# Kernel tuning notes

Measured on AMD Instinct MI355X. Metric: run time of the kernel, lower is better.

Reference implementation:

```python
import jax, jax.numpy as jnp
import numpy as np

CH = 256
B, H, W = 8, 128, 128
CQK = CH // 8


def _conv1x1(x, w, b):
    # x: [B,C,H,W], w: [O,C], b: [O]
    return jnp.einsum('bchw,oc->bohw', x, w) + b[None, :, None, None]


def setup_inputs() -> dict:
    key = jax.random.key(0)
    ks = jax.random.split(key, 8)
    sq = 1.0 / np.sqrt(CH)
    return {
        'x': jax.random.normal(ks[0], (B, CH, H, W), dtype=jnp.float32),
        'Wq': jax.random.normal(ks[1], (CQK, CH), dtype=jnp.float32) * sq,
        'bq': jax.random.normal(ks[2], (CQK,), dtype=jnp.float32) * 0.01,
        'Wk': jax.random.normal(ks[3], (CQK, CH), dtype=jnp.float32) * sq,
        'bk': jax.random.normal(ks[4], (CQK,), dtype=jnp.float32) * 0.01,
        'Wv': jax.random.normal(ks[5], (CH, CH), dtype=jnp.float32) * sq,
        'bv': jax.random.normal(ks[6], (CH,), dtype=jnp.float32) * 0.01,
        'gamma': jax.random.normal(ks[7], (1,), dtype=jnp.float32) * 0.1,
        'recurrence': 2,
    }


def reference(x, Wq, bq, Wk, bk, Wv, bv, gamma, recurrence):
    q = _conv1x1(x, Wq, bq)   # [B, C//8, H, W]
    k = _conv1x1(x, Wk, bk)   # [B, C//8, H, W]
    v = _conv1x1(x, Wv, bv)   # [B, C, H, W]
    if recurrence % 2 == 1:
        # attention along W, independently per (b, h); no mask
        energy = jnp.einsum('bchi,bchj->bhij', q, k)      # [B,H,W,W]
        att = jax.nn.softmax(energy, axis=-1)
        out = jnp.einsum('bchj,bhij->bchi', v, att)       # [B,C,H,W]
    else:
        # attention along H, independently per (b, w); diagonal masked -inf
        energy = jnp.einsum('bciw,bcjw->bwij', q, k)      # [B,W,H,H]
        h = energy.shape[-1]
        diag = jnp.eye(h, dtype=bool)[None, None]
        energy = jnp.where(diag, -jnp.inf, energy)
        att = jax.nn.softmax(energy, axis=-1)             # [B,W,H,H]
        out = jnp.einsum('bcjw,bwij->bciw', v, att)       # [B,C,H,W]
    return gamma[0] * out + x
```

## Files before the change

### kernel.cpp

```cpp
#include <hip/hip_runtime.h>
#include <hip/hip_bf16.h>

#define B_   8
#define CH_  256
#define CQK_ 32
#define H_   128
#define W_   128

typedef __attribute__((ext_vector_type(8))) short s16x8;
typedef __attribute__((ext_vector_type(4))) float f32x4;
typedef __attribute__((ext_vector_type(4))) unsigned short u16x4;

__device__ __forceinline__ unsigned short f2b(float f) {
  __hip_bfloat16 h = __float2bfloat16(f);
  return *(unsigned short*)&h;
}
__device__ __forceinline__ float b2f(unsigned short u) {
  return __uint_as_float(((unsigned)u) << 16);
}


__global__ void kw_pack(const float* __restrict__ Wq, const float* __restrict__ Wk,
                        const float* __restrict__ Wv, unsigned short* __restrict__ wqk,
                        unsigned short* __restrict__ wv) {
  int idx = blockIdx.x * 256 + threadIdx.x;
  if (idx < 64 * 256) {
    int qc = idx >> 8, c = idx & 255;
    wqk[idx] = f2b(qc < 32 ? Wq[qc * 256 + c] : Wk[(qc - 32) * 256 + c]);
  } else {
    int i2 = idx - 64 * 256;
    wv[i2] = f2b(Wv[i2]);
  }
}

__global__ __launch_bounds__(256) void k0_xpose(const float* __restrict__ x,
                                                unsigned short* __restrict__ xt) {
  __shared__ unsigned short st[256 * 137];
  const int t = threadIdx.x;
  const int b = blockIdx.x >> 7;
  const int h = blockIdx.x & 127;
  const float* xin = x + ((size_t)b * 256 * 128 + h) * 128;
  const int w = t & 127, chalf = t >> 7;
#pragma unroll 8
  for (int it = 0; it < 128; ++it) {
    int c = it * 2 + chalf;
    st[c * 137 + w] = f2b(xin[(size_t)c * 16384 + w]);
  }
  __syncthreads();
  unsigned short* xo = xt + ((size_t)b * 128 * 128 + h) * 256;
  const int cl = t & 127, whalf = t >> 7;
#pragma unroll 8
  for (int it = 0; it < 64; ++it) {
    int wr = it * 2 + whalf;
    unsigned v = (unsigned)st[(2 * cl) * 137 + wr] |
                 ((unsigned)st[(2 * cl + 1) * 137 + wr] << 16);
    *(unsigned*)&xo[(size_t)wr * 32768 + 2 * cl] = v;
  }
}

__global__ __launch_bounds__(256, 2) void k0b_xpose(const unsigned short* __restrict__ xt,
                                                    unsigned short* __restrict__ xt2) {
  __shared__ unsigned short st[128 * 264];
  const int t = threadIdx.x;
  const size_t colbase = (size_t)blockIdx.x * 32768;
#pragma unroll
  for (int it = 0; it < 16; ++it) {
    int ch = it * 256 + t;
    int row = ch >> 5, off = (ch & 31) * 8;
    *(uint4*)&st[row * 264 + off] = *(const uint4*)&xt[colbase + ch * 8];
  }
  __syncthreads();
  const int hpl = t & 3, cq = t >> 2;
#pragma unroll 8
  for (int it = 0; it < 64; ++it) {
    const int itc = it & 3, ith = it >> 2;
    const int c = itc * 64 + cq;
    const int hp = ith * 4 + hpl;
    unsigned v = (unsigned)st[(2 * hp) * 264 + c] |
                 ((unsigned)st[(2 * hp + 1) * 264 + c] << 16);
    *(unsigned*)&xt2[colbase + (size_t)c * 128 + hp * 2] = v;
  }
}

__device__ __forceinline__ void gld_lds16(const unsigned short* g, unsigned short* l) {
  __builtin_amdgcn_global_load_lds(
      (const __attribute__((address_space(1))) void*)g,
      (__attribute__((address_space(3))) void*)l, 16, 0, 0);
}

__device__ __forceinline__ void stage_tile(const unsigned short* __restrict__ gsrc,
                                           unsigned short* lds, int k0,
                                           int wv_id, int lane) {
#pragma unroll
  for (int i = 0; i < 4; ++i) {
    const int chunk = wv_id * 4 + i;
    const int L = chunk * 1024 + lane * 16;
    const int row = L >> 7;
    const int sb = L & 127;
    const int srcb = sb ^ ((row & 7) << 4);
    gld_lds16(gsrc + row * 256 + k0 + (srcb >> 1), lds + chunk * 512);
  }
}

struct SmemY {
  unsigned short qt[128 * 40];
  unsigned short kt[128 * 40];
  union {
    unsigned short att[128 * 136];
    unsigned short xstage[2][128 * 64];
  } u;
};

__global__ __launch_bounds__(256, 2)
void k1y(const unsigned short* __restrict__ xt, const unsigned short* __restrict__ xt2,
         const unsigned short* __restrict__ wqk, const float* __restrict__ bq,
         const float* __restrict__ bk, unsigned short* __restrict__ y) {
  __shared__ SmemY sm;
  const int t = threadIdx.x;
  const int wvid = t >> 6;
  const int lane = t & 63;
  const int l15 = lane & 15;
  const int quad = lane >> 4;
  const int b = blockIdx.x >> 7;
  const int w = blockIdx.x & 127;
  const size_t colbase = ((size_t)b * 128 + w) * 32768;

  {
    const int qc0 = wvid * 16;
    f32x4 acc[8];
#pragma unroll
    for (int nt = 0; nt < 8; ++nt) acc[nt] = {0.f, 0.f, 0.f, 0.f};
    const unsigned short* arow = wqk + (qc0 + l15) * 256 + quad * 8;
    const unsigned short* gcol = xt + colbase;
    stage_tile(gcol, sm.u.xstage[0], 0, wvid, lane);
    __syncthreads();
#pragma unroll
    for (int kc = 0; kc < 4; ++kc) {
      const int cur = kc & 1;
      if (kc < 3) stage_tile(gcol, sm.u.xstage[cur ^ 1], (kc + 1) * 64, wvid, lane);
#pragma unroll
      for (int kk2 = 0; kk2 < 2; ++kk2) {
        s16x8 a = *(const s16x8*)(arow + (kc * 2 + kk2) * 32);
#pragma unroll
        for (int nt = 0; nt < 8; ++nt) {
          const int row = nt * 16 + l15;
          const int col = (kk2 * 64 + quad * 16) ^ ((row & 7) << 4);
          s16x8 bb = *(const s16x8*)((const char*)sm.u.xstage[cur] + row * 128 + col);
          acc[nt] = __builtin_amdgcn_mfma_f32_16x16x32_bf16(a, bb, acc[nt], 0, 0, 0);
        }
      }
      __syncthreads();
    }
    const float* bp = (wvid < 2) ? bq : bk;
    const int qcl = qc0 & 16;
    float bias[4];
#pragma unroll
    for (int r = 0; r < 4; ++r) bias[r] = bp[qcl + quad * 4 + r];
    unsigned short* dst = (wvid < 2) ? sm.qt : sm.kt;
#pragma unroll
    for (int nt = 0; nt < 8; ++nt) {
      int h = nt * 16 + l15;
      u16x4 pk;
#pragma unroll
      for (int r = 0; r < 4; ++r) pk[r] = f2b(acc[nt][r] + bias[r]);
      *(u16x4*)&dst[h * 40 + qcl + quad * 4] = pk;
    }
  }
  __syncthreads();

  s16x8 bXpf[4][4];
  {
    const int c0 = wvid * 64;
#pragma unroll
    for (int kj = 0; kj < 4; ++kj)
#pragma unroll
      for (int nt = 0; nt < 4; ++nt)
        bXpf[kj][nt] = *(const s16x8*)&xt2[colbase + (size_t)(c0 + nt * 16 + l15) * 128 +
                                            kj * 32 + quad * 8];
  }
  __builtin_amdgcn_sched_barrier(0);

  {
    const int i0 = wvid * 32;
    s16x8 aQ[2];
#pragma unroll
    for (int mt = 0; mt < 2; ++mt)
      aQ[mt] = *(const s16x8*)&sm.qt[(i0 + mt * 16 + l15) * 40 + quad * 8];
    f32x4 eacc[2][8];
#pragma unroll
    for (int mt = 0; mt < 2; ++mt)
#pragma unroll
      for (int nt = 0; nt < 8; ++nt) eacc[mt][nt] = {0.f, 0.f, 0.f, 0.f};
#pragma unroll
    for (int nt = 0; nt < 8; ++nt) {
      s16x8 bK = *(const s16x8*)&sm.kt[(nt * 16 + l15) * 40 + quad * 8];
      eacc[0][nt] = __builtin_amdgcn_mfma_f32_16x16x32_bf16(aQ[0], bK, eacc[0][nt], 0, 0, 0);
      eacc[1][nt] = __builtin_amdgcn_mfma_f32_16x16x32_bf16(aQ[1], bK, eacc[1][nt], 0, 0, 0);
    }
#pragma unroll
    for (int mt = 0; mt < 2; ++mt)
#pragma unroll
      for (int nt = 0; nt < 8; ++nt) {
        const int j = nt * 16 + l15;
#pragma unroll
        for (int r = 0; r < 4; ++r)
          if (j == i0 + mt * 16 + quad * 4 + r) eacc[mt][nt][r] = -__builtin_inff();
      }
#pragma unroll
    for (int mt = 0; mt < 2; ++mt)
#pragma unroll
      for (int r = 0; r < 4; ++r) {
        float mx = -__builtin_inff();
#pragma unroll
        for (int nt = 0; nt < 8; ++nt) mx = fmaxf(mx, eacc[mt][nt][r]);
        mx = fmaxf(mx, __shfl_xor(mx, 1));
        mx = fmaxf(mx, __shfl_xor(mx, 2));
        mx = fmaxf(mx, __shfl_xor(mx, 4));
        mx = fmaxf(mx, __shfl_xor(mx, 8));
        float s = 0.f;
#pragma unroll
        for (int nt = 0; nt < 8; ++nt) {
          float p = __expf(eacc[mt][nt][r] - mx);
          eacc[mt][nt][r] = p;
          s += p;
        }
        s += __shfl_xor(s, 1);
        s += __shfl_xor(s, 2);
        s += __shfl_xor(s, 4);
        s += __shfl_xor(s, 8);
        const float inv = 1.0f / s;
        const int i = i0 + mt * 16 + quad * 4 + r;
#pragma unroll
        for (int nt = 0; nt < 8; ++nt)
          sm.u.att[i * 136 + nt * 16 + l15] = f2b(eacc[mt][nt][r] * inv);
      }
  }
  __syncthreads();

  f32x4 yacc[8][4];
#pragma unroll
  for (int mt = 0; mt < 8; ++mt)
#pragma unroll
    for (int nt = 0; nt < 4; ++nt) yacc[mt][nt] = {0.f, 0.f, 0.f, 0.f};
  {
#pragma unroll
    for (int kj = 0; kj < 4; ++kj) {
      s16x8 aP[8];
#pragma unroll
      for (int mt = 0; mt < 8; ++mt)
        aP[mt] = *(const s16x8*)&sm.u.att[(mt * 16 + l15) * 136 + kj * 32 + quad * 8];
#pragma unroll
      for (int nt = 0; nt < 4; ++nt) {
#pragma unroll
        for (int mt = 0; mt < 8; ++mt)
          yacc[mt][nt] = __builtin_amdgcn_mfma_f32_16x16x32_bf16(aP[mt], bXpf[kj][nt],
                                                                 yacc[mt][nt], 0, 0, 0);
      }
    }
  }
#pragma unroll 1
  for (int h2 = 0; h2 < 2; ++h2) {
    __syncthreads();
    if ((wvid >> 1) == h2) {
      const int clb = (wvid & 1) * 64;
#pragma unroll
      for (int mt = 0; mt < 8; ++mt)
#pragma unroll
        for (int nt = 0; nt < 4; ++nt) {
          const int cl = clb + nt * 16 + l15;
#pragma unroll
          for (int r = 0; r < 4; ++r)
            sm.u.att[(mt * 16 + quad * 4 + r) * 136 + cl] = f2b(yacc[mt][nt][r]);
        }
    }
    __syncthreads();
#pragma unroll
    for (int it = 0; it < 8; ++it) {
      int g = it * 256 + t;
      int i = g >> 4, cc = (g & 15) * 8;
      *(uint4*)&y[((size_t)(b * 128 + i) * 128 + w) * 256 + h2 * 128 + cc] =
          *(const uint4*)&sm.u.att[i * 136 + cc];
    }
  }
}


struct SmemG {
  unsigned short A[2][128 * 64];
  unsigned short B[2][128 * 64];
};

__global__ __launch_bounds__(256, 2)
void k2g(const unsigned short* __restrict__ y, const unsigned short* __restrict__ wv,
         const float* __restrict__ bv, const float* __restrict__ gamma,
         const float* __restrict__ x, float* __restrict__ out) {
  __shared__ SmemG sm;
  const int t = threadIdx.x;
  const int wv_id = t >> 6;
  const int lane = t & 63;
  const int l15 = lane & 15;
  const int quad = lane >> 4;
  const int mhalf = (blockIdx.x >> 3) & 1;
  const int bh = ((blockIdx.x >> 4) << 3) | (blockIdx.x & 7);
  const int b = bh >> 7, h = bh & 127;
  const unsigned short* gA = wv + mhalf * 128 * 256;
  const unsigned short* gB = y + (size_t)bh * 128 * 256;
  const int wr = wv_id >> 1;
  const int wc = wv_id & 1;

  f32x4 acc[4][4];
#pragma unroll
  for (int mt = 0; mt < 4; ++mt)
#pragma unroll
    for (int nt = 0; nt < 4; ++nt) acc[mt][nt] = {0.f, 0.f, 0.f, 0.f};
  float xpf[4][4][4];

  stage_tile(gA, sm.A[0], 0, wv_id, lane);
  stage_tile(gB, sm.B[0], 0, wv_id, lane);
  __syncthreads();

#pragma unroll
  for (int kt = 0; kt < 4; ++kt) {
    const int cur = kt & 1;
    if (kt < 3) {
      stage_tile(gA, sm.A[cur ^ 1], (kt + 1) * 64, wv_id, lane);
      stage_tile(gB, sm.B[cur ^ 1], (kt + 1) * 64, wv_id, lane);
    }
    {
      const int mt = kt;
#pragma unroll
      for (int r = 0; r < 4; ++r) {
        const int co = mhalf * 128 + wr * 64 + mt * 16 + quad * 4 + r;
        const float* xp = x + ((size_t)(b * 256 + co) * 128 + h) * 128 + wc * 64 + l15;
#pragma unroll
        for (int nt = 0; nt < 4; ++nt) xpf[mt][r][nt] = xp[nt * 16];
      }
    }
#pragma unroll
    for (int ks = 0; ks < 2; ++ks) {
      s16x8 a[4], bb[4];
#pragma unroll
      for (int mt = 0; mt < 4; ++mt) {
        const int row = wr * 64 + mt * 16 + l15;
        const int col = (ks * 64 + quad * 16) ^ ((row & 7) << 4);
        a[mt] = *(const s16x8*)((const char*)&sm.A[cur][0] + row * 128 + col);
      }
#pragma unroll
      for (int nt = 0; nt < 4; ++nt) {
        const int row = wc * 64 + nt * 16 + l15;
        const int col = (ks * 64 + quad * 16) ^ ((row & 7) << 4);
        bb[nt] = *(const s16x8*)((const char*)&sm.B[cur][0] + row * 128 + col);
      }
#pragma unroll
      for (int nt = 0; nt < 4; ++nt)
#pragma unroll
        for (int mt = 0; mt < 4; ++mt)
          acc[mt][nt] = __builtin_amdgcn_mfma_f32_16x16x32_bf16(a[mt], bb[nt], acc[mt][nt], 0, 0, 0);
    }
    __syncthreads();
  }

  const float g = gamma[0];
#pragma unroll
  for (int mt = 0; mt < 4; ++mt)
#pragma unroll
    for (int r = 0; r < 4; ++r) {
      const int co = mhalf * 128 + wr * 64 + mt * 16 + quad * 4 + r;
      const float bvv = bv[co];
      const size_t base = ((size_t)(b * 256 + co) * 128 + h) * 128;
#pragma unroll
      for (int nt = 0; nt < 4; ++nt) {
        const int wcol = wc * 64 + nt * 16 + l15;
        out[base + wcol] = g * (acc[mt][nt][r] + bvv) + xpf[mt][r][nt];
      }
    }
}


struct SmemK1 {
  __hip_bfloat16 x[CH_][H_];
  float att[H_][130];
  union {
    struct { __hip_bfloat16 q[CQK_][H_]; __hip_bfloat16 k[CQK_][H_]; } qk;
    float vchunk[32][130];
  } s;
};

__device__ __forceinline__ void load_bf16x16(const __hip_bfloat16* p, float* f) {
  const uint4* p4 = (const uint4*)p;
  uint4 a = p4[0], b = p4[1];
  unsigned uu[8] = {a.x, a.y, a.z, a.w, b.x, b.y, b.z, b.w};
#pragma unroll
  for (int m = 0; m < 8; ++m) {
    f[2 * m] = __uint_as_float(uu[m] << 16);
    f[2 * m + 1] = __uint_as_float(uu[m] & 0xffff0000u);
  }
}

__global__ __launch_bounds__(256, 1)
void k1_attn(const float* __restrict__ x, const float* __restrict__ Wq,
             const float* __restrict__ bq, const float* __restrict__ Wk,
             const float* __restrict__ bk, const float* __restrict__ Wv,
             const float* __restrict__ bv, float* __restrict__ o_t) {
  __shared__ SmemK1 sm;
  const int t = threadIdx.x;
  const int b = blockIdx.x >> 7;
  const int w = blockIdx.x & 127;
  {
    const float* xb = x + (size_t)b * CH_ * H_ * W_ + w;
    const int h = t & 127;
    const int c0 = (t >> 7) * 128;
#pragma unroll 8
    for (int r = 0; r < 128; ++r) {
      const int c = c0 + r;
      sm.x[c][h] = __float2bfloat16(xb[(size_t)(c * H_ + h) * W_]);
    }
  }
  __syncthreads();
  {
    const int qc = t >> 3;
    const int i0 = (t & 7) << 4;
    float qa[16], ka[16];
    const float bqv = bq[qc], bkv = bk[qc];
#pragma unroll
    for (int u = 0; u < 16; ++u) { qa[u] = bqv; ka[u] = bkv; }
    const float* wqr = Wq + qc * CH_;
    const float* wkr = Wk + qc * CH_;
    for (int c = 0; c < CH_; c += 4) {
      const float4 wq4 = *(const float4*)(wqr + c);
      const float4 wk4 = *(const float4*)(wkr + c);
      const float wqs[4] = {wq4.x, wq4.y, wq4.z, wq4.w};
      const float wks[4] = {wk4.x, wk4.y, wk4.z, wk4.w};
#pragma unroll
      for (int cc = 0; cc < 4; ++cc) {
        float xf[16];
        load_bf16x16(&sm.x[c + cc][i0], xf);
#pragma unroll
        for (int u = 0; u < 16; ++u) {
          qa[u] += wqs[cc] * xf[u];
          ka[u] += wks[cc] * xf[u];
        }
      }
    }
#pragma unroll
    for (int u = 0; u < 16; ++u) {
      sm.s.qk.q[qc][i0 + u] = __float2bfloat16(qa[u]);
      sm.s.qk.k[qc][i0 + u] = __float2bfloat16(ka[u]);
    }
  }
  __syncthreads();
  {
    const int i = t >> 1;
    const int j0 = (t & 1) << 6;
    float qreg[32];
#pragma unroll
    for (int qc = 0; qc < 32; ++qc) qreg[qc] = __bfloat162float(sm.s.qk.q[qc][i]);
    float e[64];
#pragma unroll
    for (int u = 0; u < 64; ++u) e[u] = 0.0f;
    for (int qc = 0; qc < 32; ++qc) {
#pragma unroll
      for (int jc = 0; jc < 4; ++jc) {
        float kf[16];
        load_bf16x16(&sm.s.qk.k[qc][j0 + jc * 16], kf);
#pragma unroll
        for (int u = 0; u < 16; ++u) e[jc * 16 + u] += qreg[qc] * kf[u];
      }
    }
    if (i >= j0 && i < j0 + 64) e[i - j0] = -__builtin_inff();
    float m = -__builtin_inff();
#pragma unroll
    for (int u = 0; u < 64; ++u) m = fmaxf(m, e[u]);
    m = fmaxf(m, __shfl_xor(m, 1));
    float ssum = 0.0f;
#pragma unroll
    for (int u = 0; u < 64; ++u) { e[u] = __expf(e[u] - m); ssum += e[u]; }
    ssum += __shfl_xor(ssum, 1);
    const float inv = 1.0f / ssum;
#pragma unroll
    for (int u = 0; u < 64; u += 2)
      *(float2*)&sm.att[i][j0 + u] = make_float2(e[u] * inv, e[u + 1] * inv);
  }
  __syncthreads();
  const int vcc = t >> 3;
  const int vj0 = (t & 7) << 4;
  const int ai0 = (t >> 3) << 2;
  const int acc0 = (t & 7) << 2;
  for (int ch = 0; ch < 8; ++ch) {
    {
      const int cg = ch * 32 + vcc;
      float acc[16];
      const float bvv = bv[cg];
#pragma unroll
      for (int u = 0; u < 16; ++u) acc[u] = bvv;
      const float* wvr = Wv + (size_t)cg * CH_;
      for (int c = 0; c < CH_; c += 4) {
        const float4 w4 = *(const float4*)(wvr + c);
        const float ws4[4] = {w4.x, w4.y, w4.z, w4.w};
#pragma unroll
        for (int cc = 0; cc < 4; ++cc) {
          float xf[16];
          load_bf16x16(&sm.x[c + cc][vj0], xf);
#pragma unroll
          for (int u = 0; u < 16; ++u) acc[u] += ws4[cc] * xf[u];
        }
      }
#pragma unroll
      for (int m2 = 0; m2 < 8; ++m2)
        *(float2*)&sm.s.vchunk[vcc][vj0 + 2 * m2] = make_float2(acc[2 * m2], acc[2 * m2 + 1]);
    }
    __syncthreads();
    {
      float oacc[4][4];
#pragma unroll
      for (int s2 = 0; s2 < 4; ++s2)
#pragma unroll
        for (int u = 0; u < 4; ++u) oacc[s2][u] = 0.0f;
#pragma unroll 4
      for (int j = 0; j < H_; j += 2) {
        float2 av[4], vv[4];
#pragma unroll
        for (int u = 0; u < 4; ++u) av[u] = *(const float2*)&sm.att[ai0 + u][j];
#pragma unroll
        for (int s2 = 0; s2 < 4; ++s2) vv[s2] = *(const float2*)&sm.s.vchunk[acc0 + s2][j];
#pragma unroll
        for (int s2 = 0; s2 < 4; ++s2)
#pragma unroll
          for (int u = 0; u < 4; ++u)
            oacc[s2][u] += vv[s2].x * av[u].x + vv[s2].y * av[u].y;
      }
#pragma unroll
      for (int s2 = 0; s2 < 4; ++s2) {
        const int cg = ch * 32 + acc0 + s2;
        float4 st;
        st.x = oacc[s2][0]; st.y = oacc[s2][1]; st.z = oacc[s2][2]; st.w = oacc[s2][3];
        *(float4*)&o_t[(((size_t)b * CH_ + cg) * W_ + w) * H_ + ai0] = st;
      }
    }
    __syncthreads();
  }
}

__global__ __launch_bounds__(256)
void k2_epi(const float* __restrict__ o_t, const float* __restrict__ x,
            const float* __restrict__ gamma, float* __restrict__ out) {
  const int pr = blockIdx.x % 10;
  const int plane = blockIdx.x / 10;
  const int rT[10] = {0, 0, 0, 0, 1, 1, 1, 2, 2, 3};
  const int sT[10] = {0, 1, 2, 3, 1, 2, 3, 2, 3, 3};
  const int r = rT[pr], s = sT[pr];
  __shared__ float t1[32][33];
  __shared__ float t2[32][33];
  const int t = threadIdx.x;
  const size_t pbase = (size_t)plane * (H_ * W_);
  const float* ob = o_t + pbase;
#pragma unroll
  for (int ii = 0; ii < 4; ++ii) {
    const int idx = ii * 256 + t;
    const int ww = idx >> 5, hh = idx & 31;
    t1[ww][hh] = ob[(s * 32 + ww) * H_ + (r * 32 + hh)];
    if (r != s) t2[ww][hh] = ob[(r * 32 + ww) * H_ + (s * 32 + hh)];
  }
  __syncthreads();
  const float g = gamma[0];
#pragma unroll
  for (int ii = 0; ii < 4; ++ii) {
    const int idx = ii * 256 + t;
    const int hh = idx >> 5, ww = idx & 31;
    const size_t o1 = pbase + (size_t)(r * 32 + hh) * W_ + (s * 32 + ww);
    out[o1] = g * t1[ww][hh] + x[o1];
    if (r != s) {
      const size_t o2 = pbase + (size_t)(s * 32 + hh) * W_ + (r * 32 + ww);
      out[o2] = g * t2[ww][hh] + x[o2];
    }
  }
}


extern "C" void kernel_launch(void* const* d_in, const int* in_sizes, int n_in,
                              void* d_out, int out_size, void* d_ws, size_t ws_size,
                              hipStream_t stream) {
  const float* x     = (const float*)d_in[0];
  const float* Wq    = (const float*)d_in[1];
  const float* bq    = (const float*)d_in[2];
  const float* Wk    = (const float*)d_in[3];
  const float* bk    = (const float*)d_in[4];
  const float* Wv    = (const float*)d_in[5];
  const float* bv    = (const float*)d_in[6];
  const float* gamma = (const float*)d_in[7];
  float* out = (float*)d_out;

  const size_t XT   = (size_t)B_ * W_ * H_ * CH_ * 2;
  const size_t YT   = XT;
  const size_t WQKB = 64 * 256 * 2;
  const size_t WVB  = 256 * 256 * 2;
  const size_t FAST_WS = XT + YT + WQKB + WVB;

  if (ws_size >= FAST_WS) {
    unsigned short* xt  = (unsigned short*)d_ws;
    unsigned short* yb  = (unsigned short*)((char*)d_ws + XT);
    unsigned short* wqk = (unsigned short*)((char*)d_ws + XT + YT);
    unsigned short* wvb = (unsigned short*)((char*)d_ws + XT + YT + WQKB);
    unsigned short* xt2 = (unsigned short*)d_out;
    hipLaunchKernelGGL(kw_pack, dim3(320), dim3(256), 0, stream, Wq, Wk, Wv, wqk, wvb);
    hipLaunchKernelGGL(k0_xpose, dim3(B_ * H_), dim3(256), 0, stream, x, xt);
    hipLaunchKernelGGL(k0b_xpose, dim3(B_ * W_), dim3(256), 0, stream, xt, xt2);
    hipLaunchKernelGGL(k1y, dim3(B_ * W_), dim3(256), 0, stream,
                       xt, xt2, wqk, bq, bk, yb);
    hipLaunchKernelGGL(k2g, dim3(B_ * H_ * 2), dim3(256), 0, stream,
                       yb, wvb, bv, gamma, x, out);
  } else {
    const size_t OT_F = (size_t)B_ * CH_ * H_ * W_ * sizeof(float);
    float* o_t = (ws_size >= OT_F) ? (float*)d_ws : out;
    hipLaunchKernelGGL(k1_attn, dim3(B_ * W_), dim3(256), 0, stream,
                       x, Wq, bq, Wk, bk, Wv, bv, o_t);
    hipLaunchKernelGGL(k2_epi, dim3((B_ * CH_) * 10), dim3(256), 0, stream,
                       o_t, x, gamma, out);
  }
}
```

Before: 373.3 us.

## Drop second transpose kernel; gather transposed X fragments from staged LDS tiles

Measured after the change: 343.4 us. 1.09x faster.

```diff
diff --git a/kernel.cpp b/kernel.cpp
--- a/kernel.cpp
+++ b/kernel.cpp
@@ -58,30 +58,6 @@
   }
 }
 
-__global__ __launch_bounds__(256, 2) void k0b_xpose(const unsigned short* __restrict__ xt,
-                                                    unsigned short* __restrict__ xt2) {
-  __shared__ unsigned short st[128 * 264];
-  const int t = threadIdx.x;
-  const size_t colbase = (size_t)blockIdx.x * 32768;
-#pragma unroll
-  for (int it = 0; it < 16; ++it) {
-    int ch = it * 256 + t;
-    int row = ch >> 5, off = (ch & 31) * 8;
-    *(uint4*)&st[row * 264 + off] = *(const uint4*)&xt[colbase + ch * 8];
-  }
-  __syncthreads();
-  const int hpl = t & 3, cq = t >> 2;
-#pragma unroll 8
-  for (int it = 0; it < 64; ++it) {
-    const int itc = it & 3, ith = it >> 2;
-    const int c = itc * 64 + cq;
-    const int hp = ith * 4 + hpl;
-    unsigned v = (unsigned)st[(2 * hp) * 264 + c] |
-                 ((unsigned)st[(2 * hp + 1) * 264 + c] << 16);
-    *(unsigned*)&xt2[colbase + (size_t)c * 128 + hp * 2] = v;
-  }
-}
-
 __device__ __forceinline__ void gld_lds16(const unsigned short* g, unsigned short* l) {
   __builtin_amdgcn_global_load_lds(
       (const __attribute__((address_space(1))) void*)g,
@@ -112,9 +88,9 @@
 };
 
 __global__ __launch_bounds__(256, 2)
-void k1y(const unsigned short* __restrict__ xt, const unsigned short* __restrict__ xt2,
-         const unsigned short* __restrict__ wqk, const float* __restrict__ bq,
-         const float* __restrict__ bk, unsigned short* __restrict__ y) {
+void k1y(const unsigned short* __restrict__ xt, const unsigned short* __restrict__ wqk,
+         const float* __restrict__ bq, const float* __restrict__ bk,
+         unsigned short* __restrict__ y) {
   __shared__ SmemY sm;
   const int t = threadIdx.x;
   const int wvid = t >> 6;
@@ -125,6 +101,8 @@
   const int w = blockIdx.x & 127;
   const size_t colbase = ((size_t)b * 128 + w) * 32768;
 
+  s16x8 bXpf[4][4];
+
   {
     const int qc0 = wvid * 16;
     f32x4 acc[8];
@@ -138,6 +116,20 @@
     for (int kc = 0; kc < 4; ++kc) {
       const int cur = kc & 1;
       if (kc < 3) stage_tile(gcol, sm.u.xstage[cur ^ 1], (kc + 1) * 64, wvid, lane);
+      if (kc == wvid) {
+        const char* chunkp = (const char*)sm.u.xstage[cur];
+#pragma unroll
+        for (int kj = 0; kj < 4; ++kj)
+#pragma unroll
+          for (int nt = 0; nt < 4; ++nt)
+#pragma unroll
+            for (int e = 0; e < 8; ++e) {
+              const int row = kj * 32 + quad * 8 + e;
+              const int cb = ((nt * 16 + l15) * 2) ^ ((row & 7) << 4);
+              bXpf[kj][nt][e] =
+                  *(const short*)(chunkp + row * 128 + cb);
+            }
+      }
 #pragma unroll
       for (int kk2 = 0; kk2 < 2; ++kk2) {
         s16x8 a = *(const s16x8*)(arow + (kc * 2 + kk2) * 32);
@@ -167,18 +159,6 @@
     }
   }
   __syncthreads();
-
-  s16x8 bXpf[4][4];
-  {
-    const int c0 = wvid * 64;
-#pragma unroll
-    for (int kj = 0; kj < 4; ++kj)
-#pragma unroll
-      for (int nt = 0; nt < 4; ++nt)
-        bXpf[kj][nt] = *(const s16x8*)&xt2[colbase + (size_t)(c0 + nt * 16 + l15) * 128 +
-                                            kj * 32 + quad * 8];
-  }
-  __builtin_amdgcn_sched_barrier(0);
 
   {
     const int i0 = wvid * 32;
@@ -601,12 +581,10 @@
     unsigned short* yb  = (unsigned short*)((char*)d_ws + XT);
     unsigned short* wqk = (unsigned short*)((char*)d_ws + XT + YT);
     unsigned short* wvb = (unsigned short*)((char*)d_ws + XT + YT + WQKB);
-    unsigned short* xt2 = (unsigned short*)d_out;
     hipLaunchKernelGGL(kw_pack, dim3(320), dim3(256), 0, stream, Wq, Wk, Wv, wqk, wvb);
     hipLaunchKernelGGL(k0_xpose, dim3(B_ * H_), dim3(256), 0, stream, x, xt);
-    hipLaunchKernelGGL(k0b_xpose, dim3(B_ * W_), dim3(256), 0, stream, xt, xt2);
     hipLaunchKernelGGL(k1y, dim3(B_ * W_), dim3(256), 0, stream,
-                       xt, xt2, wqk, bq, bk, yb);
+                       xt, wqk, bq, bk, yb);
     hipLaunchKernelGGL(k2g, dim3(B_ * H_ * 2), dim3(256), 0, stream,
                        yb, wvb, bv, gamma, x, out);
   } else {
```
